# Optimization experiments

Measured on AMD Instinct MI355X. Metric: run time of the kernel, lower is better.

Reference implementation:

```python
import jax, jax.numpy as jnp
import numpy as np

NEG_SLOPE = 0.2  # PyG GATConv default negative_slope


def _gat_dense(x, W, att_src, att_dst, bias):
    """PyG GATConv on a fully-connected graph (self-loops included) == dense attention.
    x: [N, F_in], W: [F_in, H*C], att_src/att_dst: [H, C], bias: [H*C] or [C].
    Returns per-head outputs [N, H, C] (bias added by caller after concat/mean).
    """
    H, C = att_src.shape
    N = x.shape[0]
    h = (x @ W).reshape(N, H, C)                      # transformed node feats
    s = jnp.einsum('nhc,hc->nh', h, att_src)          # alpha_src per source node
    t = jnp.einsum('nhc,hc->nh', h, att_dst)          # alpha_dst per dest node
    # e[i, j, h] = leaky_relu(alpha_dst[i] + alpha_src[j]); softmax over sources j
    e = jax.nn.leaky_relu(t[:, None, :] + s[None, :, :], NEG_SLOPE)  # [N, N, H]
    a = jax.nn.softmax(e, axis=1)
    out = jnp.einsum('ijh,jhc->ihc', a, h)            # aggregate sources -> dest
    return out


def setup_inputs() -> dict:
    key = jax.random.key(0)
    ks = jax.random.split(key, 11)
    N, D, C, H = 4096, 768, 128, 4
    sd1 = 1.0 / np.sqrt(D)
    sd2 = 1.0 / np.sqrt(H * C)
    sd3 = 1.0 / np.sqrt(C)
    return {
        'node_feats': jax.random.normal(ks[0], (N, D), dtype=jnp.float32),
        'W1': jax.random.normal(ks[1], (D, H * C), dtype=jnp.float32) * sd1,
        'att_src1': jax.random.normal(ks[2], (H, C), dtype=jnp.float32) * sd3,
        'att_dst1': jax.random.normal(ks[3], (H, C), dtype=jnp.float32) * sd3,
        'b1': jnp.zeros((H * C,), dtype=jnp.float32),
        'W2': jax.random.normal(ks[4], (H * C, C), dtype=jnp.float32) * sd2,
        'att_src2': jax.random.normal(ks[5], (1, C), dtype=jnp.float32) * sd3,
        'att_dst2': jax.random.normal(ks[6], (1, C), dtype=jnp.float32) * sd3,
        'b2': jnp.zeros((C,), dtype=jnp.float32),
        'fcW': jax.random.normal(ks[7], (C, D), dtype=jnp.float32) * sd3,
        'fcb': jnp.zeros((D,), dtype=jnp.float32),
    }


def reference(node_feats, W1, att_src1, att_dst1, b1, W2, att_src2, att_dst2, b2, fcW, fcb):
    N = node_feats.shape[0]
    # GAT layer 1: 4 heads, concat=True
    x = _gat_dense(node_feats, W1, att_src1, att_dst1, b1).reshape(N, -1) + b1
    x = jax.nn.elu(x)
    # GAT layer 2: 1 head, concat=False (mean over the single head == identity)
    x = _gat_dense(x, W2, att_src2, att_dst2, b2)[:, 0, :] + b2
    x = jax.nn.elu(x)
    x = x.mean(axis=0)            # [gat_hidden]
    return x @ fcW + fcb          # [hidden_dim]
```

## Files before the change

kernel.cpp:

```cpp
#include <hip/hip_runtime.h>
#include <hip/hip_bf16.h>


#define NNODE 4096
#define CDIM 128
#define TW 132
#define NEG 0.2f
#define CHUNK 32
#define NCHUNK 128

typedef __bf16 bf16x8 __attribute__((ext_vector_type(8)));
typedef float f32x4 __attribute__((ext_vector_type(4)));

__device__ __forceinline__ unsigned short f2b(float f) {
  unsigned int u = __float_as_uint(f);
  u += 0x7fffu + ((u >> 16) & 1u);
  return (unsigned short)(u >> 16);
}

__global__ __launch_bounds__(256) void prep_kernel(const float* __restrict__ x,
                                                   const float* __restrict__ W1,
                                                   const float* __restrict__ W2,
                                                   unsigned short* __restrict__ xb,
                                                   unsigned short* __restrict__ W1t,
                                                   unsigned short* __restrict__ W2t,
                                                   float* __restrict__ zs1,
                                                   float* __restrict__ zs2) {
  __shared__ float tile[64][65];
  int b = blockIdx.x, t = threadIdx.x;
  if (b < 3072) {
    int i = b * 256 + t;
    float4 v = ((const float4*)x)[i];
    ushort4 o;
    o.x = f2b(v.x); o.y = f2b(v.y); o.z = f2b(v.z); o.w = f2b(v.w);
    ((ushort4*)xb)[i] = o;
    return;
  }
  if (b >= 3184) {
    float4 z = {0.f, 0.f, 0.f, 0.f};
    if (b < 3216) {
      ((float4*)zs1)[(b - 3184) * 256 + t] = z;
    } else {
      ((float4*)zs2)[(b - 3216) * 256 + t] = z;
    }
    return;
  }
  const float* W; unsigned short* Wt; int K, N, n0, k0;
  if (b < 3072 + 96) {
    int b2 = b - 3072; W = W1; Wt = W1t; K = 768; N = 512;
    n0 = (b2 & 7) * 64; k0 = (b2 >> 3) * 64;
  } else {
    int b3 = b - 3072 - 96; W = W2; Wt = W2t; K = 512; N = 128;
    n0 = (b3 & 1) * 64; k0 = (b3 >> 1) * 64;
  }
  for (int p = 0; p < 16; p++) {
    int e = p * 256 + t;
    int rr = e >> 6, cc = e & 63;
    tile[rr][cc] = W[(size_t)(k0 + rr) * N + n0 + cc];
  }
  __syncthreads();
  for (int p = 0; p < 16; p++) {
    int e = p * 256 + t;
    int rr = e >> 6, cc = e & 63;
    Wt[(size_t)(n0 + rr) * K + k0 + cc] = f2b(tile[cc][rr]);
  }
}

template <int BM, int BN>
__global__ __launch_bounds__(256) void mfma_gemm_bt(const unsigned short* __restrict__ A,
                                                    const unsigned short* __restrict__ Bt,
                                                    float* __restrict__ C,
                                                    int M, int N, int K,
                                                    float* __restrict__ sAcc,
                                                    float* __restrict__ tAcc,
                                                    const float* __restrict__ av_s,
                                                    const float* __restrict__ av_d) {
  __shared__ __align__(16) unsigned short As[BM * 40];
  __shared__ __align__(16) unsigned short Bs[BN * 40];
  constexpr int WM = BM / 2, WN = BN / 2;
  constexpr int FI = WM / 16, FJ = WN / 16;
  constexpr int EA = BM * 32 / 8;
  constexpr int EB = BN * 32 / 8;
  constexpr int NA = (EA + 255) / 256;
  constexpr int NB = (EB + 255) / 256;
  int tid = threadIdx.x;
  int lane = tid & 63, wave = tid >> 6;
  int wm = (wave >> 1) * WM, wn = (wave & 1) * WN;
  int m0 = blockIdx.y * BM, n0 = blockIdx.x * BN;
  int fm = lane & 15, fq = lane >> 4;
  f32x4 acc[FI][FJ] = {};
  uint4 ar[NA], br[NB];
#pragma unroll
  for (int q = 0; q < NA; q++) {
    int e = q * 256 + tid;
    if (e < EA) {
      int r = e >> 2, kk = (e & 3) * 8;
      ar[q] = *(const uint4*)(A + (size_t)(m0 + r) * K + kk);
    }
  }
#pragma unroll
  for (int q = 0; q < NB; q++) {
    int e = q * 256 + tid;
    if (e < EB) {
      int r = e >> 2, kk = (e & 3) * 8;
      br[q] = *(const uint4*)(Bt + (size_t)(n0 + r) * K + kk);
    }
  }
  for (int k0 = 0; k0 < K; k0 += 32) {
    __syncthreads();
#pragma unroll
    for (int q = 0; q < NA; q++) {
      int e = q * 256 + tid;
      if (e < EA) {
        int r = e >> 2, kk = (e & 3) * 8;
        *(uint4*)&As[r * 40 + kk] = ar[q];
      }
    }
#pragma unroll
    for (int q = 0; q < NB; q++) {
      int e = q * 256 + tid;
      if (e < EB) {
        int r = e >> 2, kk = (e & 3) * 8;
        *(uint4*)&Bs[r * 40 + kk] = br[q];
      }
    }
    __syncthreads();
    if (k0 + 32 < K) {
#pragma unroll
      for (int q = 0; q < NA; q++) {
        int e = q * 256 + tid;
        if (e < EA) {
          int r = e >> 2, kk = (e & 3) * 8;
          ar[q] = *(const uint4*)(A + (size_t)(m0 + r) * K + k0 + 32 + kk);
        }
      }
#pragma unroll
      for (int q = 0; q < NB; q++) {
        int e = q * 256 + tid;
        if (e < EB) {
          int r = e >> 2, kk = (e & 3) * 8;
          br[q] = *(const uint4*)(Bt + (size_t)(n0 + r) * K + k0 + 32 + kk);
        }
      }
    }
    bf16x8 af[FI], bfr[FJ];
#pragma unroll
    for (int i = 0; i < FI; i++)
      af[i] = *(const bf16x8*)&As[(wm + i * 16 + fm) * 40 + fq * 8];
#pragma unroll
    for (int j = 0; j < FJ; j++)
      bfr[j] = *(const bf16x8*)&Bs[(wn + j * 16 + fm) * 40 + fq * 8];
#pragma unroll
    for (int i = 0; i < FI; i++)
#pragma unroll
      for (int j = 0; j < FJ; j++)
        acc[i][j] = __builtin_amdgcn_mfma_f32_16x16x32_bf16(af[i], bfr[j], acc[i][j], 0, 0, 0);
  }
#pragma unroll
  for (int i = 0; i < FI; i++) {
#pragma unroll
    for (int j = 0; j < FJ; j++) {
      int r = m0 + wm + i * 16 + fq * 4;
      int ccol = n0 + wn + j * 16 + fm;
#pragma unroll
      for (int reg = 0; reg < 4; reg++)
        C[(size_t)(r + reg) * N + ccol] = acc[i][j][reg];
    }
  }
  {
    int hh = n0 >> 7;
    float avs[FJ], avd[FJ];
#pragma unroll
    for (int j = 0; j < FJ; j++) {
      int col = n0 + wn + j * 16 + fm;
      avs[j] = av_s[col];
      avd[j] = av_d[col];
    }
#pragma unroll
    for (int i = 0; i < FI; i++) {
#pragma unroll
      for (int reg = 0; reg < 4; reg++) {
        float sv = 0.f, tv = 0.f;
#pragma unroll
        for (int j = 0; j < FJ; j++) {
          sv = fmaf(acc[i][j][reg], avs[j], sv);
          tv = fmaf(acc[i][j][reg], avd[j], tv);
        }
#pragma unroll
        for (int o = 1; o < 16; o <<= 1) {
          sv += __shfl_xor(sv, o, 64);
          tv += __shfl_xor(tv, o, 64);
        }
        if (fm == 0) {
          int row = m0 + wm + i * 16 + fq * 4 + reg;
          atomicAdd(&sAcc[(size_t)hh * NNODE + row], sv);
          atomicAdd(&tAcc[(size_t)hh * NNODE + row], tv);
        }
      }
    }
  }
}

__global__ __launch_bounds__(256) void rank_sort_kernel(const float* __restrict__ s,
                                                        const float* __restrict__ t,
                                                        float* __restrict__ ss,
                                                        int* __restrict__ si,
                                                        int* __restrict__ qlo) {
  __shared__ __align__(16) float keys[NNODE];
  __shared__ int pc[8][32], qc[8][32];
  int hh = blockIdx.y, tid = threadIdx.x;
  const float* sp = s + (size_t)hh * NNODE;
  for (int k = tid; k < NNODE / 4; k += 256)
    ((float4*)keys)[k] = ((const float4*)sp)[k];
  __syncthreads();
  int slot = tid & 31, part = tid >> 5;
  int node = blockIdx.x * 32 + slot;
  float mk = keys[node];
  float qk = -t[(size_t)hh * NNODE + node];
  int cnt = 0, cq = 0;
  int j0 = part * 512;
#pragma unroll 4
  for (int j = j0; j < j0 + 512; j += 4) {
    float4 kv = *(const float4*)&keys[j];
    cnt += (kv.x < mk) || (kv.x == mk && (j + 0) < node);
    cnt += (kv.y < mk) || (kv.y == mk && (j + 1) < node);
    cnt += (kv.z < mk) || (kv.z == mk && (j + 2) < node);
    cnt += (kv.w < mk) || (kv.w == mk && (j + 3) < node);
    cq += (kv.x < qk) + (kv.y < qk) + (kv.z < qk) + (kv.w < qk);
  }
  pc[part][slot] = cnt;
  qc[part][slot] = cq;
  __syncthreads();
  if (tid < 32) {
    int rank = 0;
#pragma unroll
    for (int p = 0; p < 8; p++) rank += pc[p][tid];
    int n2 = blockIdx.x * 32 + tid;
    ss[(size_t)hh * NNODE + rank] = keys[n2];
    si[(size_t)hh * NNODE + rank] = n2;
  } else if (tid < 64) {
    int sl = tid - 32;
    int lo = 0;
#pragma unroll
    for (int p = 0; p < 8; p++) lo += qc[p][sl];
    qlo[(size_t)hh * NNODE + blockIdx.x * 32 + sl] = lo;
  }
}

__global__ __launch_bounds__(128) void passA_kernel(const float* __restrict__ h,
                                                    const float* __restrict__ ss,
                                                    const int* __restrict__ si,
                                                    float* __restrict__ partP,
                                                    float* __restrict__ partM, int H) {
  __shared__ float eP[CHUNK], eM[CHUNK];
  __shared__ int ids[CHUNK];
  int b = blockIdx.x, hh = b / NCHUNK, ci = b % NCHUNK;
  int c = threadIdx.x;
  int HC = H * CDIM;
  int base = ci * CHUNK;
  if (c < CHUNK) {
    float sv = ss[(size_t)hh * NNODE + base + c];
    ids[c] = si[(size_t)hh * NNODE + base + c];
    eP[c] = expf(sv);
    eM[c] = expf(NEG * sv);
  }
  __syncthreads();
  float sp = 0.f, sm = 0.f;
  for (int kb = 0; kb < CHUNK; kb += 8) {
    float v[8];
#pragma unroll
    for (int j = 0; j < 8; j++)
      v[j] = h[(size_t)ids[kb + j] * HC + hh * CDIM + c];
#pragma unroll
    for (int j = 0; j < 8; j++) {
      sp = fmaf(eP[kb + j], v[j], sp);
      sm = fmaf(eM[kb + j], v[j], sm);
    }
  }
  size_t o = ((size_t)hh * NCHUNK + ci) * TW;
  partP[o + c] = sp;
  partM[o + c] = sm;
  if (c == 0) {
    float zp = 0.f, zm = 0.f;
#pragma unroll
    for (int k = 0; k < CHUNK; k++) { zp += eP[k]; zm += eM[k]; }
    partP[o + 128] = zp;
    partM[o + 128] = zm;
  }
}

__global__ __launch_bounds__(192) void passB_kernel(const float* __restrict__ partP,
                                                    const float* __restrict__ partM,
                                                    float* __restrict__ sufP,
                                                    float* __restrict__ prefM) {
  int hh = blockIdx.y, dir = blockIdx.x;
  int c = threadIdx.x;
  if (c > 128) return;
  size_t base = (size_t)hh * NCHUNK * TW;
  if (dir == 0) {
    float run = 0.f;
    for (int g0 = 0; g0 < NCHUNK; g0 += 8) {
      float v[8];
#pragma unroll
      for (int j = 0; j < 8; j++) v[j] = partM[base + (size_t)(g0 + j) * TW + c];
#pragma unroll
      for (int j = 0; j < 8; j++) {
        prefM[base + (size_t)(g0 + j) * TW + c] = run;
        run += v[j];
      }
    }
  } else {
    float run = 0.f;
    for (int g0 = NCHUNK - 8; g0 >= 0; g0 -= 8) {
      float v[8];
#pragma unroll
      for (int j = 7; j >= 0; j--) v[j] = partP[base + (size_t)(g0 + j) * TW + c];
#pragma unroll
      for (int j = 7; j >= 0; j--) {
        sufP[base + (size_t)(g0 + j) * TW + c] = run;
        run += v[j];
      }
    }
  }
}

__global__ __launch_bounds__(128) void passC_kernel(const float* __restrict__ h,
                                                    const float* __restrict__ ss,
                                                    const int* __restrict__ si,
                                                    const float* __restrict__ sufP,
                                                    const float* __restrict__ prefM,
                                                    float* __restrict__ SS,
                                                    float* __restrict__ PP, int H) {
  __shared__ float hrow[CHUNK][CDIM];
  __shared__ float eP[CHUNK], eM[CHUNK];
  __shared__ int ids[CHUNK];
  int b = blockIdx.x, hh = b / NCHUNK, ci = b % NCHUNK;
  int c = threadIdx.x;
  int HC = H * CDIM;
  int base = ci * CHUNK;
  size_t hb = (size_t)hh * (NNODE + 1);
  if (c < CHUNK) {
    float sv = ss[(size_t)hh * NNODE + base + c];
    ids[c] = si[(size_t)hh * NNODE + base + c];
    eP[c] = expf(sv);
    eM[c] = expf(NEG * sv);
  }
  __syncthreads();
  size_t co = ((size_t)hh * NCHUNK + ci) * TW;
  float cm = prefM[co + c];
  float cp = sufP[co + c];
  float zcm = 0.f, zcp = 0.f;
  if (c == 0) { zcm = prefM[co + 128]; zcp = sufP[co + 128]; }
  for (int kb = 0; kb < CHUNK; kb += 8) {
    float v[8];
#pragma unroll
    for (int j = 0; j < 8; j++)
      v[j] = h[(size_t)ids[kb + j] * HC + hh * CDIM + c];
#pragma unroll
    for (int j = 0; j < 8; j++) hrow[kb + j][c] = v[j];
  }
  float runm = cm, runzm = zcm;
#pragma unroll 8
  for (int k = 0; k < CHUNK; k++) {
    size_t row = (hb + base + k) * TW;
    PP[row + c] = runm;
    if (c == 0) PP[row + 128] = runzm;
    runm = fmaf(eM[k], hrow[k][c], runm);
    runzm += eM[k];
  }
  if (ci == NCHUNK - 1) {
    size_t row = (hb + NNODE) * TW;
    PP[row + c] = runm;
    if (c == 0) PP[row + 128] = runzm;
  }
  float runp = cp, runzp = zcp;
#pragma unroll 8
  for (int k = CHUNK - 1; k >= 0; k--) {
    runp = fmaf(eP[k], hrow[k][c], runp);
    runzp += eP[k];
    size_t row = (hb + base + k) * TW;
    SS[row + c] = runp;
    if (c == 0) SS[row + 128] = runzp;
  }
  if (ci == NCHUNK - 1) {
    size_t row = (hb + NNODE) * TW;
    SS[row + c] = 0.f;
    if (c == 0) SS[row + 128] = 0.f;
  }
}

template <typename OUT>
__global__ __launch_bounds__(128) void attend_kernel(const float* __restrict__ SS,
                                                     const float* __restrict__ PP,
                                                     const int* __restrict__ qlo,
                                                     const float* __restrict__ tt,
                                                     const float* __restrict__ bias,
                                                     OUT* __restrict__ out, int H) {
  int b = blockIdx.x;
  int n = b / H, hh = b % H;
  int c = threadIdx.x;
  float tv = tt[(size_t)hh * NNODE + n];
  int lo = qlo[(size_t)hh * NNODE + n];
  size_t hb = (size_t)hh * (NNODE + 1);
  float wp = expf(tv), wm = expf(NEG * tv);
  float num = wp * SS[(hb + lo) * TW + c] + wm * PP[(hb + lo) * TW + c];
  float Z = wp * SS[(hb + lo) * TW + 128] + wm * PP[(hb + lo) * TW + 128];
  float o = num / Z + bias[hh * CDIM + c];
  float r = (o > 0.f) ? o : (expf(o) - 1.f);
  if constexpr (sizeof(OUT) == 2)
    out[(size_t)n * (H * CDIM) + hh * CDIM + c] = f2b(r);
  else
    out[(size_t)n * (H * CDIM) + hh * CDIM + c] = r;
}

__global__ __launch_bounds__(256) void mean_part_kernel(const float* __restrict__ x,
                                                        float* __restrict__ part) {
  __shared__ float4 red[256];
  int b = blockIdx.x, tid = threadIdx.x;
  int q = tid & 31, r0 = tid >> 5;
  const float4* xp = (const float4*)x;
  float4 s = {0.f, 0.f, 0.f, 0.f};
  int base = b * 64;
  for (int r = r0; r < 64; r += 8) {
    float4 v = xp[(size_t)(base + r) * 32 + q];
    s.x += v.x; s.y += v.y; s.z += v.z; s.w += v.w;
  }
  red[tid] = s; __syncthreads();
  for (int off = 4; off > 0; off >>= 1) {
    if (r0 < off) {
      float4 o = red[tid + off * 32];
      red[tid].x += o.x; red[tid].y += o.y; red[tid].z += o.z; red[tid].w += o.w;
    }
    __syncthreads();
  }
  if (tid < 32) ((float4*)part)[b * 32 + tid] = red[tid];
}

__global__ __launch_bounds__(256) void fc_kernel(const float* __restrict__ part,
                                                 const float* __restrict__ fcW,
                                                 const float* __restrict__ fcb,
                                                 float* __restrict__ out) {
  __shared__ float tmp[256];
  __shared__ float m[CDIM];
  int tid = threadIdx.x;
  int c = tid & 127, half = tid >> 7;
  float a = 0.f;
  for (int g = half; g < 64; g += 2) a += part[g * CDIM + c];
  tmp[tid] = a; __syncthreads();
  if (tid < 128) m[tid] = (tmp[tid] + tmp[tid + 128]) * (1.f / NNODE);
  __syncthreads();
  int d = blockIdx.x * 256 + tid;
  float acc = fcb[d];
#pragma unroll 4
  for (int c2 = 0; c2 < CDIM; c2++) acc = fmaf(m[c2], fcW[c2 * 768 + d], acc);
  out[d] = acc;
}

extern "C" void kernel_launch(void* const* d_in, const int* in_sizes, int n_in,
                              void* d_out, int out_size, void* d_ws, size_t ws_size,
                              hipStream_t stream) {
  const float* x   = (const float*)d_in[0];
  const float* W1  = (const float*)d_in[1];
  const float* as1 = (const float*)d_in[2];
  const float* ad1 = (const float*)d_in[3];
  const float* b1  = (const float*)d_in[4];
  const float* W2  = (const float*)d_in[5];
  const float* as2 = (const float*)d_in[6];
  const float* ad2 = (const float*)d_in[7];
  const float* b2  = (const float*)d_in[8];
  const float* fcW = (const float*)d_in[9];
  const float* fcb = (const float*)d_in[10];

  float* ws = (float*)d_ws;
  size_t off = 0;
  auto alloc = [&](size_t nfloats) { float* p = ws + off; off += nfloats; return p; };

  float* h1  = alloc((size_t)NNODE * 512);
  float* x2f = alloc((size_t)NNODE * 256 + 64 + 16384);
  float* h2  = alloc((size_t)NNODE * 128);
  float* x3  = alloc((size_t)NNODE * 128);
  float* s1  = alloc((size_t)4 * NNODE);
  float* t1  = alloc((size_t)4 * NNODE);
  float* sS1 = alloc((size_t)4 * NNODE);
  int*   sI1 = (int*)alloc((size_t)4 * NNODE);
  int*   qL1 = (int*)alloc((size_t)4 * NNODE);
  float* SS1 = alloc((size_t)4 * (NNODE + 1) * TW);
  float* PP1 = alloc((size_t)4 * (NNODE + 1) * TW);
  float* pP1 = alloc((size_t)4 * NCHUNK * TW);
  float* pM1 = alloc((size_t)4 * NCHUNK * TW);
  float* fP1 = alloc((size_t)4 * NCHUNK * TW);
  float* fM1 = alloc((size_t)4 * NCHUNK * TW);
  float* s2  = alloc(NNODE);
  float* t2  = alloc(NNODE);
  float* sS2 = alloc(NNODE);
  int*   sI2 = (int*)alloc(NNODE);
  int*   qL2 = (int*)alloc(NNODE);
  float* SS2 = alloc((size_t)(NNODE + 1) * TW);
  float* PP2 = alloc((size_t)(NNODE + 1) * TW);
  float* pP2 = alloc((size_t)NCHUNK * TW);
  float* pM2 = alloc((size_t)NCHUNK * TW);
  float* fP2 = alloc((size_t)NCHUNK * TW);
  float* fM2 = alloc((size_t)NCHUNK * TW);
  float* mpart = alloc((size_t)64 * CDIM);

  unsigned short* xb  = (unsigned short*)PP1;
  unsigned short* W1t = (unsigned short*)SS1;
  unsigned short* x2b = (unsigned short*)x2f;
  unsigned short* W2t = (unsigned short*)(x2f + NNODE * 256 + 64);

  prep_kernel<<<3224, 256, 0, stream>>>(x, W1, W2, xb, W1t, W2t, s1, s2);
  mfma_gemm_bt<64, 64><<<dim3(512 / 64, NNODE / 64), 256, 0, stream>>>(
      xb, W1t, h1, NNODE, 512, 768, s1, t1, as1, ad1);
  rank_sort_kernel<<<dim3(NNODE / 32, 4), 256, 0, stream>>>(s1, t1, sS1, sI1, qL1);
  passA_kernel<<<4 * NCHUNK, 128, 0, stream>>>(h1, sS1, sI1, pP1, pM1, 4);
  passB_kernel<<<dim3(2, 4), 192, 0, stream>>>(pP1, pM1, fP1, fM1);
  passC_kernel<<<4 * NCHUNK, 128, 0, stream>>>(h1, sS1, sI1, fP1, fM1, SS1, PP1, 4);
  attend_kernel<unsigned short><<<NNODE * 4, 128, 0, stream>>>(SS1, PP1, qL1, t1, b1, x2b, 4);
  mfma_gemm_bt<32, 64><<<dim3(128 / 64, NNODE / 32), 256, 0, stream>>>(
      x2b, W2t, h2, NNODE, 128, 512, s2, t2, as2, ad2);
  rank_sort_kernel<<<dim3(NNODE / 32, 1), 256, 0, stream>>>(s2, t2, sS2, sI2, qL2);
  passA_kernel<<<NCHUNK, 128, 0, stream>>>(h2, sS2, sI2, pP2, pM2, 1);
  passB_kernel<<<dim3(2, 1), 192, 0, stream>>>(pP2, pM2, fP2, fM2);
  passC_kernel<<<NCHUNK, 128, 0, stream>>>(h2, sS2, sI2, fP2, fM2, SS2, PP2, 1);
  attend_kernel<float><<<NNODE, 128, 0, stream>>>(SS2, PP2, qL2, t2, b2, x3, 1);
  mean_part_kernel<<<64, 256, 0, stream>>>(x3, mpart);
  fc_kernel<<<3, 256, 0, stream>>>(mpart, fcW, fcb, (float*)d_out);
}
```

Measured before the change: 209.6 us.

## Fuse per-layer attention stages into one cooperative kernel with grid syncs

Replaces the separate rank-sort, pass A/B/C, attend, mean and fc launches of each GAT layer with a single cooperative kernel of 512 blocks that uses grid.sync between stages and a shared-memory union. The aim is to remove many small kernel launches and their gaps. Work is also repacked into 256-thread blocks: pass A handles two chunks per block, pass C splits the prefix and suffix scans across half-blocks, and attend loops over several nodes per block. In exchange, idle blocks have to wait at grid barriers. The fixed 512-block grid must be fully co-resident for the cooperative launch to run.

```diff
diff --git a/kernel.cpp b/kernel.cpp
--- a/kernel.cpp
+++ b/kernel.cpp
@@ -1,5 +1,8 @@
 #include <hip/hip_runtime.h>
 #include <hip/hip_bf16.h>
+#include <hip/hip_cooperative_groups.h>
+
+namespace cg = cooperative_groups;
 
 
 #define NNODE 4096
@@ -8,6 +11,7 @@
 #define NEG 0.2f
 #define CHUNK 32
 #define NCHUNK 128
+#define CGRID 512
 
 typedef __bf16 bf16x8 __attribute__((ext_vector_type(8)));
 typedef float f32x4 __attribute__((ext_vector_type(4)));
@@ -201,259 +205,256 @@
   }
 }
 
-__global__ __launch_bounds__(256) void rank_sort_kernel(const float* __restrict__ s,
-                                                        const float* __restrict__ t,
-                                                        float* __restrict__ ss,
-                                                        int* __restrict__ si,
-                                                        int* __restrict__ qlo) {
-  __shared__ __align__(16) float keys[NNODE];
-  __shared__ int pc[8][32], qc[8][32];
-  int hh = blockIdx.y, tid = threadIdx.x;
-  const float* sp = s + (size_t)hh * NNODE;
-  for (int k = tid; k < NNODE / 4; k += 256)
-    ((float4*)keys)[k] = ((const float4*)sp)[k];
-  __syncthreads();
-  int slot = tid & 31, part = tid >> 5;
-  int node = blockIdx.x * 32 + slot;
-  float mk = keys[node];
-  float qk = -t[(size_t)hh * NNODE + node];
-  int cnt = 0, cq = 0;
-  int j0 = part * 512;
+struct SmSort { float keys[NNODE]; int pc[8][32]; int qc[8][32]; };
+struct SmA    { float eP[2][CHUNK]; float eM[2][CHUNK]; int ids[2][CHUNK]; };
+struct SmC    { float hrow[CHUNK][CDIM]; float eP[CHUNK]; float eM[CHUNK]; int ids[CHUNK]; };
+struct SmM    { float4 red[256]; };
+struct SmF    { float tmp[256]; float m[CDIM]; };
+union SmU { SmSort srt; SmA pa; SmC pc; SmM mp; SmF fc; };
+
+template <int H, typename OUT, bool READOUT>
+__global__ __launch_bounds__(256) void layer_coop(
+    const float* __restrict__ h,
+    const float* __restrict__ sv, const float* __restrict__ tvv,
+    float* __restrict__ ss, int* __restrict__ si, int* __restrict__ qlo,
+    float* __restrict__ pP, float* __restrict__ pM,
+    float* __restrict__ fP, float* __restrict__ fM,
+    float* __restrict__ SS, float* __restrict__ PP,
+    const float* __restrict__ bias, OUT* __restrict__ outp,
+    const float* __restrict__ fcW, const float* __restrict__ fcb,
+    float* __restrict__ mpart, float* __restrict__ fcout) {
+  __shared__ __align__(16) SmU sm;
+  cg::grid_group grid = cg::this_grid();
+  int b = blockIdx.x, tid = threadIdx.x;
+  constexpr int HC = H * CDIM;
+
+  if (b < H * 128) {
+    int hh = b >> 7, sb = b & 127;
+    const float* sp = sv + (size_t)hh * NNODE;
+    for (int k = tid; k < NNODE / 4; k += 256)
+      ((float4*)sm.srt.keys)[k] = ((const float4*)sp)[k];
+    __syncthreads();
+    int slot = tid & 31, part = tid >> 5;
+    int node = sb * 32 + slot;
+    float mk = sm.srt.keys[node];
+    float qk = -tvv[(size_t)hh * NNODE + node];
+    int cnt = 0, cq = 0;
+    int j0 = part * 512;
 #pragma unroll 4
-  for (int j = j0; j < j0 + 512; j += 4) {
-    float4 kv = *(const float4*)&keys[j];
-    cnt += (kv.x < mk) || (kv.x == mk && (j + 0) < node);
-    cnt += (kv.y < mk) || (kv.y == mk && (j + 1) < node);
-    cnt += (kv.z < mk) || (kv.z == mk && (j + 2) < node);
-    cnt += (kv.w < mk) || (kv.w == mk && (j + 3) < node);
-    cq += (kv.x < qk) + (kv.y < qk) + (kv.z < qk) + (kv.w < qk);
-  }
-  pc[part][slot] = cnt;
-  qc[part][slot] = cq;
-  __syncthreads();
-  if (tid < 32) {
-    int rank = 0;
-#pragma unroll
-    for (int p = 0; p < 8; p++) rank += pc[p][tid];
-    int n2 = blockIdx.x * 32 + tid;
-    ss[(size_t)hh * NNODE + rank] = keys[n2];
-    si[(size_t)hh * NNODE + rank] = n2;
-  } else if (tid < 64) {
-    int sl = tid - 32;
-    int lo = 0;
-#pragma unroll
-    for (int p = 0; p < 8; p++) lo += qc[p][sl];
-    qlo[(size_t)hh * NNODE + blockIdx.x * 32 + sl] = lo;
-  }
-}
-
-__global__ __launch_bounds__(128) void passA_kernel(const float* __restrict__ h,
-                                                    const float* __restrict__ ss,
-                                                    const int* __restrict__ si,
-                                                    float* __restrict__ partP,
-                                                    float* __restrict__ partM, int H) {
-  __shared__ float eP[CHUNK], eM[CHUNK];
-  __shared__ int ids[CHUNK];
-  int b = blockIdx.x, hh = b / NCHUNK, ci = b % NCHUNK;
-  int c = threadIdx.x;
-  int HC = H * CDIM;
-  int base = ci * CHUNK;
-  if (c < CHUNK) {
-    float sv = ss[(size_t)hh * NNODE + base + c];
-    ids[c] = si[(size_t)hh * NNODE + base + c];
-    eP[c] = expf(sv);
-    eM[c] = expf(NEG * sv);
-  }
-  __syncthreads();
-  float sp = 0.f, sm = 0.f;
-  for (int kb = 0; kb < CHUNK; kb += 8) {
-    float v[8];
-#pragma unroll
-    for (int j = 0; j < 8; j++)
-      v[j] = h[(size_t)ids[kb + j] * HC + hh * CDIM + c];
-#pragma unroll
-    for (int j = 0; j < 8; j++) {
-      sp = fmaf(eP[kb + j], v[j], sp);
-      sm = fmaf(eM[kb + j], v[j], sm);
-    }
-  }
-  size_t o = ((size_t)hh * NCHUNK + ci) * TW;
-  partP[o + c] = sp;
-  partM[o + c] = sm;
-  if (c == 0) {
-    float zp = 0.f, zm = 0.f;
-#pragma unroll
-    for (int k = 0; k < CHUNK; k++) { zp += eP[k]; zm += eM[k]; }
-    partP[o + 128] = zp;
-    partM[o + 128] = zm;
-  }
-}
-
-__global__ __launch_bounds__(192) void passB_kernel(const float* __restrict__ partP,
-                                                    const float* __restrict__ partM,
-                                                    float* __restrict__ sufP,
-                                                    float* __restrict__ prefM) {
-  int hh = blockIdx.y, dir = blockIdx.x;
-  int c = threadIdx.x;
-  if (c > 128) return;
-  size_t base = (size_t)hh * NCHUNK * TW;
-  if (dir == 0) {
-    float run = 0.f;
-    for (int g0 = 0; g0 < NCHUNK; g0 += 8) {
+    for (int j = j0; j < j0 + 512; j += 4) {
+      float4 kv = *(const float4*)&sm.srt.keys[j];
+      cnt += (kv.x < mk) || (kv.x == mk && (j + 0) < node);
+      cnt += (kv.y < mk) || (kv.y == mk && (j + 1) < node);
+      cnt += (kv.z < mk) || (kv.z == mk && (j + 2) < node);
+      cnt += (kv.w < mk) || (kv.w == mk && (j + 3) < node);
+      cq += (kv.x < qk) + (kv.y < qk) + (kv.z < qk) + (kv.w < qk);
+    }
+    sm.srt.pc[part][slot] = cnt;
+    sm.srt.qc[part][slot] = cq;
+    __syncthreads();
+    if (tid < 32) {
+      int rank = 0;
+#pragma unroll
+      for (int p = 0; p < 8; p++) rank += sm.srt.pc[p][tid];
+      int n2 = sb * 32 + tid;
+      ss[(size_t)hh * NNODE + rank] = sm.srt.keys[n2];
+      si[(size_t)hh * NNODE + rank] = n2;
+    } else if (tid < 64) {
+      int sl = tid - 32;
+      int lo = 0;
+#pragma unroll
+      for (int p = 0; p < 8; p++) lo += sm.srt.qc[p][sl];
+      qlo[(size_t)hh * NNODE + sb * 32 + sl] = lo;
+    }
+  }
+  grid.sync();
+
+  if (b < H * (NCHUNK / 2)) {
+    int half = tid >> 7, c = tid & 127;
+    int hh = b / (NCHUNK / 2), pair = b % (NCHUNK / 2);
+    int ci = pair * 2 + half;
+    int base = ci * CHUNK;
+    if (c < CHUNK) {
+      float s0 = ss[(size_t)hh * NNODE + base + c];
+      sm.pa.ids[half][c] = si[(size_t)hh * NNODE + base + c];
+      sm.pa.eP[half][c] = expf(s0);
+      sm.pa.eM[half][c] = expf(NEG * s0);
+    }
+    __syncthreads();
+    float sp = 0.f, smm = 0.f;
+    for (int kb = 0; kb < CHUNK; kb += 8) {
       float v[8];
 #pragma unroll
-      for (int j = 0; j < 8; j++) v[j] = partM[base + (size_t)(g0 + j) * TW + c];
+      for (int j = 0; j < 8; j++)
+        v[j] = h[(size_t)sm.pa.ids[half][kb + j] * HC + hh * CDIM + c];
 #pragma unroll
       for (int j = 0; j < 8; j++) {
-        prefM[base + (size_t)(g0 + j) * TW + c] = run;
-        run += v[j];
-      }
-    }
-  } else {
-    float run = 0.f;
-    for (int g0 = NCHUNK - 8; g0 >= 0; g0 -= 8) {
+        sp = fmaf(sm.pa.eP[half][kb + j], v[j], sp);
+        smm = fmaf(sm.pa.eM[half][kb + j], v[j], smm);
+      }
+    }
+    size_t o = ((size_t)hh * NCHUNK + ci) * TW;
+    pP[o + c] = sp;
+    pM[o + c] = smm;
+    if (c == 0) {
+      float zp = 0.f, zm = 0.f;
+#pragma unroll
+      for (int k = 0; k < CHUNK; k++) { zp += sm.pa.eP[half][k]; zm += sm.pa.eM[half][k]; }
+      pP[o + 128] = zp;
+      pM[o + 128] = zm;
+    }
+  }
+  grid.sync();
+
+  if (b < 2 * H && tid <= 128) {
+    int hh = b >> 1, dir = b & 1;
+    int c = tid;
+    size_t base = (size_t)hh * NCHUNK * TW;
+    if (dir == 0) {
+      float run = 0.f;
+      for (int g0 = 0; g0 < NCHUNK; g0 += 8) {
+        float v[8];
+#pragma unroll
+        for (int j = 0; j < 8; j++) v[j] = pM[base + (size_t)(g0 + j) * TW + c];
+#pragma unroll
+        for (int j = 0; j < 8; j++) {
+          fM[base + (size_t)(g0 + j) * TW + c] = run;
+          run += v[j];
+        }
+      }
+    } else {
+      float run = 0.f;
+      for (int g0 = NCHUNK - 8; g0 >= 0; g0 -= 8) {
+        float v[8];
+#pragma unroll
+        for (int j = 7; j >= 0; j--) v[j] = pP[base + (size_t)(g0 + j) * TW + c];
+#pragma unroll
+        for (int j = 7; j >= 0; j--) {
+          fP[base + (size_t)(g0 + j) * TW + c] = run;
+          run += v[j];
+        }
+      }
+    }
+  }
+  grid.sync();
+
+  if (b < H * NCHUNK) {
+    int hh = b / NCHUNK, ci = b % NCHUNK;
+    int c = tid & 127, half = tid >> 7;
+    int base = ci * CHUNK;
+    size_t hb = (size_t)hh * (NNODE + 1);
+    if (tid < CHUNK) {
+      float s0 = ss[(size_t)hh * NNODE + base + tid];
+      sm.pc.ids[tid] = si[(size_t)hh * NNODE + base + tid];
+      sm.pc.eP[tid] = expf(s0);
+      sm.pc.eM[tid] = expf(NEG * s0);
+    }
+    __syncthreads();
+    for (int kb = half * 16; kb < half * 16 + 16; kb += 8) {
       float v[8];
 #pragma unroll
-      for (int j = 7; j >= 0; j--) v[j] = partP[base + (size_t)(g0 + j) * TW + c];
-#pragma unroll
-      for (int j = 7; j >= 0; j--) {
-        sufP[base + (size_t)(g0 + j) * TW + c] = run;
-        run += v[j];
-      }
-    }
-  }
-}
-
-__global__ __launch_bounds__(128) void passC_kernel(const float* __restrict__ h,
-                                                    const float* __restrict__ ss,
-                                                    const int* __restrict__ si,
-                                                    const float* __restrict__ sufP,
-                                                    const float* __restrict__ prefM,
-                                                    float* __restrict__ SS,
-                                                    float* __restrict__ PP, int H) {
-  __shared__ float hrow[CHUNK][CDIM];
-  __shared__ float eP[CHUNK], eM[CHUNK];
-  __shared__ int ids[CHUNK];
-  int b = blockIdx.x, hh = b / NCHUNK, ci = b % NCHUNK;
-  int c = threadIdx.x;
-  int HC = H * CDIM;
-  int base = ci * CHUNK;
-  size_t hb = (size_t)hh * (NNODE + 1);
-  if (c < CHUNK) {
-    float sv = ss[(size_t)hh * NNODE + base + c];
-    ids[c] = si[(size_t)hh * NNODE + base + c];
-    eP[c] = expf(sv);
-    eM[c] = expf(NEG * sv);
-  }
-  __syncthreads();
-  size_t co = ((size_t)hh * NCHUNK + ci) * TW;
-  float cm = prefM[co + c];
-  float cp = sufP[co + c];
-  float zcm = 0.f, zcp = 0.f;
-  if (c == 0) { zcm = prefM[co + 128]; zcp = sufP[co + 128]; }
-  for (int kb = 0; kb < CHUNK; kb += 8) {
-    float v[8];
-#pragma unroll
-    for (int j = 0; j < 8; j++)
-      v[j] = h[(size_t)ids[kb + j] * HC + hh * CDIM + c];
-#pragma unroll
-    for (int j = 0; j < 8; j++) hrow[kb + j][c] = v[j];
-  }
-  float runm = cm, runzm = zcm;
+      for (int j = 0; j < 8; j++)
+        v[j] = h[(size_t)sm.pc.ids[kb + j] * HC + hh * CDIM + c];
+#pragma unroll
+      for (int j = 0; j < 8; j++) sm.pc.hrow[kb + j][c] = v[j];
+    }
+    __syncthreads();
+    size_t co = ((size_t)hh * NCHUNK + ci) * TW;
+    if (half == 0) {
+      float runm = fM[co + c];
+      float runzm = (c == 0) ? fM[co + 128] : 0.f;
 #pragma unroll 8
-  for (int k = 0; k < CHUNK; k++) {
-    size_t row = (hb + base + k) * TW;
-    PP[row + c] = runm;
-    if (c == 0) PP[row + 128] = runzm;
-    runm = fmaf(eM[k], hrow[k][c], runm);
-    runzm += eM[k];
-  }
-  if (ci == NCHUNK - 1) {
-    size_t row = (hb + NNODE) * TW;
-    PP[row + c] = runm;
-    if (c == 0) PP[row + 128] = runzm;
-  }
-  float runp = cp, runzp = zcp;
+      for (int k = 0; k < CHUNK; k++) {
+        size_t row = (hb + base + k) * TW;
+        PP[row + c] = runm;
+        if (c == 0) PP[row + 128] = runzm;
+        runm = fmaf(sm.pc.eM[k], sm.pc.hrow[k][c], runm);
+        runzm += sm.pc.eM[k];
+      }
+      if (ci == NCHUNK - 1) {
+        size_t row = (hb + NNODE) * TW;
+        PP[row + c] = runm;
+        if (c == 0) PP[row + 128] = runzm;
+      }
+    } else {
+      float runp = fP[co + c];
+      float runzp = (c == 0) ? fP[co + 128] : 0.f;
 #pragma unroll 8
-  for (int k = CHUNK - 1; k >= 0; k--) {
-    runp = fmaf(eP[k], hrow[k][c], runp);
-    runzp += eP[k];
-    size_t row = (hb + base + k) * TW;
-    SS[row + c] = runp;
-    if (c == 0) SS[row + 128] = runzp;
-  }
-  if (ci == NCHUNK - 1) {
-    size_t row = (hb + NNODE) * TW;
-    SS[row + c] = 0.f;
-    if (c == 0) SS[row + 128] = 0.f;
-  }
-}
-
-template <typename OUT>
-__global__ __launch_bounds__(128) void attend_kernel(const float* __restrict__ SS,
-                                                     const float* __restrict__ PP,
-                                                     const int* __restrict__ qlo,
-                                                     const float* __restrict__ tt,
-                                                     const float* __restrict__ bias,
-                                                     OUT* __restrict__ out, int H) {
-  int b = blockIdx.x;
-  int n = b / H, hh = b % H;
-  int c = threadIdx.x;
-  float tv = tt[(size_t)hh * NNODE + n];
-  int lo = qlo[(size_t)hh * NNODE + n];
-  size_t hb = (size_t)hh * (NNODE + 1);
-  float wp = expf(tv), wm = expf(NEG * tv);
-  float num = wp * SS[(hb + lo) * TW + c] + wm * PP[(hb + lo) * TW + c];
-  float Z = wp * SS[(hb + lo) * TW + 128] + wm * PP[(hb + lo) * TW + 128];
-  float o = num / Z + bias[hh * CDIM + c];
-  float r = (o > 0.f) ? o : (expf(o) - 1.f);
-  if constexpr (sizeof(OUT) == 2)
-    out[(size_t)n * (H * CDIM) + hh * CDIM + c] = f2b(r);
-  else
-    out[(size_t)n * (H * CDIM) + hh * CDIM + c] = r;
-}
-
-__global__ __launch_bounds__(256) void mean_part_kernel(const float* __restrict__ x,
-                                                        float* __restrict__ part) {
-  __shared__ float4 red[256];
-  int b = blockIdx.x, tid = threadIdx.x;
-  int q = tid & 31, r0 = tid >> 5;
-  const float4* xp = (const float4*)x;
-  float4 s = {0.f, 0.f, 0.f, 0.f};
-  int base = b * 64;
-  for (int r = r0; r < 64; r += 8) {
-    float4 v = xp[(size_t)(base + r) * 32 + q];
-    s.x += v.x; s.y += v.y; s.z += v.z; s.w += v.w;
-  }
-  red[tid] = s; __syncthreads();
-  for (int off = 4; off > 0; off >>= 1) {
-    if (r0 < off) {
-      float4 o = red[tid + off * 32];
-      red[tid].x += o.x; red[tid].y += o.y; red[tid].z += o.z; red[tid].w += o.w;
-    }
-    __syncthreads();
-  }
-  if (tid < 32) ((float4*)part)[b * 32 + tid] = red[tid];
-}
-
-__global__ __launch_bounds__(256) void fc_kernel(const float* __restrict__ part,
-                                                 const float* __restrict__ fcW,
-                                                 const float* __restrict__ fcb,
-                                                 float* __restrict__ out) {
-  __shared__ float tmp[256];
-  __shared__ float m[CDIM];
-  int tid = threadIdx.x;
-  int c = tid & 127, half = tid >> 7;
-  float a = 0.f;
-  for (int g = half; g < 64; g += 2) a += part[g * CDIM + c];
-  tmp[tid] = a; __syncthreads();
-  if (tid < 128) m[tid] = (tmp[tid] + tmp[tid + 128]) * (1.f / NNODE);
-  __syncthreads();
-  int d = blockIdx.x * 256 + tid;
-  float acc = fcb[d];
+      for (int k = CHUNK - 1; k >= 0; k--) {
+        runp = fmaf(sm.pc.eP[k], sm.pc.hrow[k][c], runp);
+        runzp += sm.pc.eP[k];
+        size_t row = (hb + base + k) * TW;
+        SS[row + c] = runp;
+        if (c == 0) SS[row + 128] = runzp;
+      }
+      if (ci == NCHUNK - 1) {
+        size_t row = (hb + NNODE) * TW;
+        SS[row + c] = 0.f;
+        if (c == 0) SS[row + 128] = 0.f;
+      }
+    }
+  }
+  grid.sync();
+
+  {
+    constexpr int PER = (H * NNODE) / CGRID;
+    int half = tid >> 7, c = tid & 127;
+#pragma unroll 2
+    for (int it = 0; it < PER / 2; it++) {
+      int o = b * PER + it * 2 + half;
+      int n = o / H, hh = o % H;
+      float tv = tvv[(size_t)hh * NNODE + n];
+      int lo = qlo[(size_t)hh * NNODE + n];
+      size_t hb = (size_t)hh * (NNODE + 1);
+      float wp = expf(tv), wm = expf(NEG * tv);
+      float num = wp * SS[(hb + lo) * TW + c] + wm * PP[(hb + lo) * TW + c];
+      float Z = wp * SS[(hb + lo) * TW + 128] + wm * PP[(hb + lo) * TW + 128];
+      float ov = num / Z + bias[hh * CDIM + c];
+      float r = (ov > 0.f) ? ov : (expf(ov) - 1.f);
+      if constexpr (sizeof(OUT) == 2)
+        outp[(size_t)n * HC + hh * CDIM + c] = f2b(r);
+      else
+        outp[(size_t)n * HC + hh * CDIM + c] = r;
+    }
+  }
+
+  if constexpr (READOUT) {
+    grid.sync();
+    if (b < 64) {
+      int q = tid & 31, r0 = tid >> 5;
+      const float4* xp = (const float4*)outp;
+      float4 s4 = {0.f, 0.f, 0.f, 0.f};
+      int base = b * 64;
+      for (int r = r0; r < 64; r += 8) {
+        float4 v = xp[(size_t)(base + r) * 32 + q];
+        s4.x += v.x; s4.y += v.y; s4.z += v.z; s4.w += v.w;
+      }
+      sm.mp.red[tid] = s4; __syncthreads();
+      for (int off = 4; off > 0; off >>= 1) {
+        if (r0 < off) {
+          float4 o4 = sm.mp.red[tid + off * 32];
+          sm.mp.red[tid].x += o4.x; sm.mp.red[tid].y += o4.y;
+          sm.mp.red[tid].z += o4.z; sm.mp.red[tid].w += o4.w;
+        }
+        __syncthreads();
+      }
+      if (tid < 32) ((float4*)mpart)[b * 32 + tid] = sm.mp.red[tid];
+    }
+    grid.sync();
+    if (b < 3) {
+      int c = tid & 127, hf = tid >> 7;
+      float a = 0.f;
+      for (int g = hf; g < 64; g += 2) a += mpart[g * CDIM + c];
+      sm.fc.tmp[tid] = a; __syncthreads();
+      if (tid < 128) sm.fc.m[tid] = (sm.fc.tmp[tid] + sm.fc.tmp[tid + 128]) * (1.f / NNODE);
+      __syncthreads();
+      int d = b * 256 + tid;
+      float acc = fcb[d];
 #pragma unroll 4
-  for (int c2 = 0; c2 < CDIM; c2++) acc = fmaf(m[c2], fcW[c2 * 768 + d], acc);
-  out[d] = acc;
+      for (int c2 = 0; c2 < CDIM; c2++) acc = fmaf(sm.fc.m[c2], fcW[c2 * 768 + d], acc);
+      fcout[d] = acc;
+    }
+  }
 }
 
 extern "C" void kernel_launch(void* const* d_in, const int* in_sizes, int n_in,
@@ -507,22 +508,27 @@
   unsigned short* W1t = (unsigned short*)SS1;
   unsigned short* x2b = (unsigned short*)x2f;
   unsigned short* W2t = (unsigned short*)(x2f + NNODE * 256 + 64);
+  float* dout = (float*)d_out;
 
   prep_kernel<<<3224, 256, 0, stream>>>(x, W1, W2, xb, W1t, W2t, s1, s2);
   mfma_gemm_bt<64, 64><<<dim3(512 / 64, NNODE / 64), 256, 0, stream>>>(
       xb, W1t, h1, NNODE, 512, 768, s1, t1, as1, ad1);
-  rank_sort_kernel<<<dim3(NNODE / 32, 4), 256, 0, stream>>>(s1, t1, sS1, sI1, qL1);
-  passA_kernel<<<4 * NCHUNK, 128, 0, stream>>>(h1, sS1, sI1, pP1, pM1, 4);
-  passB_kernel<<<dim3(2, 4), 192, 0, stream>>>(pP1, pM1, fP1, fM1);
-  passC_kernel<<<4 * NCHUNK, 128, 0, stream>>>(h1, sS1, sI1, fP1, fM1, SS1, PP1, 4);
-  attend_kernel<unsigned short><<<NNODE * 4, 128, 0, stream>>>(SS1, PP1, qL1, t1, b1, x2b, 4);
+  {
+    auto* kfn = layer_coop<4, unsigned short, false>;
+    void* ka[] = {(void*)&h1, (void*)&s1, (void*)&t1, (void*)&sS1, (void*)&sI1,
+                  (void*)&qL1, (void*)&pP1, (void*)&pM1, (void*)&fP1, (void*)&fM1,
+                  (void*)&SS1, (void*)&PP1, (void*)&b1, (void*)&x2b,
+                  (void*)&fcW, (void*)&fcb, (void*)&mpart, (void*)&dout};
+    hipLaunchCooperativeKernel((const void*)kfn, dim3(CGRID), dim3(256), ka, 0, stream);
+  }
   mfma_gemm_bt<32, 64><<<dim3(128 / 64, NNODE / 32), 256, 0, stream>>>(
       x2b, W2t, h2, NNODE, 128, 512, s2, t2, as2, ad2);
-  rank_sort_kernel<<<dim3(NNODE / 32, 1), 256, 0, stream>>>(s2, t2, sS2, sI2, qL2);
-  passA_kernel<<<NCHUNK, 128, 0, stream>>>(h2, sS2, sI2, pP2, pM2, 1);
-  passB_kernel<<<dim3(2, 1), 192, 0, stream>>>(pP2, pM2, fP2, fM2);
-  passC_kernel<<<NCHUNK, 128, 0, stream>>>(h2, sS2, sI2, fP2, fM2, SS2, PP2, 1);
-  attend_kernel<float><<<NNODE, 128, 0, stream>>>(SS2, PP2, qL2, t2, b2, x3, 1);
-  mean_part_kernel<<<64, 256, 0, stream>>>(x3, mpart);
-  fc_kernel<<<3, 256, 0, stream>>>(mpart, fcW, fcb, (float*)d_out);
+  {
+    auto* kfn = layer_coop<1, float, true>;
+    void* ka[] = {(void*)&h2, (void*)&s2, (void*)&t2, (void*)&sS2, (void*)&sI2,
+                  (void*)&qL2, (void*)&pP2, (void*)&pM2, (void*)&fP2, (void*)&fM2,
+                  (void*)&SS2, (void*)&PP2, (void*)&b2, (void*)&x3,
+                  (void*)&fcW, (void*)&fcb, (void*)&mpart, (void*)&dout};
+    hipLaunchCooperativeKernel((const void*)kfn, dim3(CGRID), dim3(256), ka, 0, stream);
+  }
 }
```

Result: slower. 753.6 us (+259.5%).

## Fuse chunk-local scans with partial sums and add chunk offsets in attend

Applied to the files above, without the earlier changes.

Merges passA and passC into one kernel. It writes chunk-local prefix and suffix scans together with the per-chunk totals, so the gather of h rows happens once instead of twice. The cross-chunk offsets from passB are now added inside attend_kernel, which reads two more small vectors per output. attend_kernel also processes two (node, head) pairs per 256-thread block, halving the block count. This removes a full kernel launch and a second gather pass, at the cost of extra loads in attend.

```diff
diff --git a/kernel.cpp b/kernel.cpp
--- a/kernel.cpp
+++ b/kernel.cpp
@@ -247,90 +247,13 @@
   }
 }
 
-__global__ __launch_bounds__(128) void passA_kernel(const float* __restrict__ h,
-                                                    const float* __restrict__ ss,
-                                                    const int* __restrict__ si,
-                                                    float* __restrict__ partP,
-                                                    float* __restrict__ partM, int H) {
-  __shared__ float eP[CHUNK], eM[CHUNK];
-  __shared__ int ids[CHUNK];
-  int b = blockIdx.x, hh = b / NCHUNK, ci = b % NCHUNK;
-  int c = threadIdx.x;
-  int HC = H * CDIM;
-  int base = ci * CHUNK;
-  if (c < CHUNK) {
-    float sv = ss[(size_t)hh * NNODE + base + c];
-    ids[c] = si[(size_t)hh * NNODE + base + c];
-    eP[c] = expf(sv);
-    eM[c] = expf(NEG * sv);
-  }
-  __syncthreads();
-  float sp = 0.f, sm = 0.f;
-  for (int kb = 0; kb < CHUNK; kb += 8) {
-    float v[8];
-#pragma unroll
-    for (int j = 0; j < 8; j++)
-      v[j] = h[(size_t)ids[kb + j] * HC + hh * CDIM + c];
-#pragma unroll
-    for (int j = 0; j < 8; j++) {
-      sp = fmaf(eP[kb + j], v[j], sp);
-      sm = fmaf(eM[kb + j], v[j], sm);
-    }
-  }
-  size_t o = ((size_t)hh * NCHUNK + ci) * TW;
-  partP[o + c] = sp;
-  partM[o + c] = sm;
-  if (c == 0) {
-    float zp = 0.f, zm = 0.f;
-#pragma unroll
-    for (int k = 0; k < CHUNK; k++) { zp += eP[k]; zm += eM[k]; }
-    partP[o + 128] = zp;
-    partM[o + 128] = zm;
-  }
-}
-
-__global__ __launch_bounds__(192) void passB_kernel(const float* __restrict__ partP,
-                                                    const float* __restrict__ partM,
-                                                    float* __restrict__ sufP,
-                                                    float* __restrict__ prefM) {
-  int hh = blockIdx.y, dir = blockIdx.x;
-  int c = threadIdx.x;
-  if (c > 128) return;
-  size_t base = (size_t)hh * NCHUNK * TW;
-  if (dir == 0) {
-    float run = 0.f;
-    for (int g0 = 0; g0 < NCHUNK; g0 += 8) {
-      float v[8];
-#pragma unroll
-      for (int j = 0; j < 8; j++) v[j] = partM[base + (size_t)(g0 + j) * TW + c];
-#pragma unroll
-      for (int j = 0; j < 8; j++) {
-        prefM[base + (size_t)(g0 + j) * TW + c] = run;
-        run += v[j];
-      }
-    }
-  } else {
-    float run = 0.f;
-    for (int g0 = NCHUNK - 8; g0 >= 0; g0 -= 8) {
-      float v[8];
-#pragma unroll
-      for (int j = 7; j >= 0; j--) v[j] = partP[base + (size_t)(g0 + j) * TW + c];
-#pragma unroll
-      for (int j = 7; j >= 0; j--) {
-        sufP[base + (size_t)(g0 + j) * TW + c] = run;
-        run += v[j];
-      }
-    }
-  }
-}
-
-__global__ __launch_bounds__(128) void passC_kernel(const float* __restrict__ h,
-                                                    const float* __restrict__ ss,
-                                                    const int* __restrict__ si,
-                                                    const float* __restrict__ sufP,
-                                                    const float* __restrict__ prefM,
-                                                    float* __restrict__ SS,
-                                                    float* __restrict__ PP, int H) {
+__global__ __launch_bounds__(128) void passAC_kernel(const float* __restrict__ h,
+                                                     const float* __restrict__ ss,
+                                                     const int* __restrict__ si,
+                                                     float* __restrict__ partP,
+                                                     float* __restrict__ partM,
+                                                     float* __restrict__ SS,
+                                                     float* __restrict__ PP, int H) {
   __shared__ float hrow[CHUNK][CDIM];
   __shared__ float eP[CHUNK], eM[CHUNK];
   __shared__ int ids[CHUNK];
@@ -346,11 +269,6 @@
     eM[c] = expf(NEG * sv);
   }
   __syncthreads();
-  size_t co = ((size_t)hh * NCHUNK + ci) * TW;
-  float cm = prefM[co + c];
-  float cp = sufP[co + c];
-  float zcm = 0.f, zcp = 0.f;
-  if (c == 0) { zcm = prefM[co + 128]; zcp = sufP[co + 128]; }
   for (int kb = 0; kb < CHUNK; kb += 8) {
     float v[8];
 #pragma unroll
@@ -359,7 +277,7 @@
 #pragma unroll
     for (int j = 0; j < 8; j++) hrow[kb + j][c] = v[j];
   }
-  float runm = cm, runzm = zcm;
+  float runm = 0.f, runzm = 0.f;
 #pragma unroll 8
   for (int k = 0; k < CHUNK; k++) {
     size_t row = (hb + base + k) * TW;
@@ -368,12 +286,15 @@
     runm = fmaf(eM[k], hrow[k][c], runm);
     runzm += eM[k];
   }
+  size_t o = ((size_t)hh * NCHUNK + ci) * TW;
+  partM[o + c] = runm;
+  if (c == 0) partM[o + 128] = runzm;
   if (ci == NCHUNK - 1) {
     size_t row = (hb + NNODE) * TW;
     PP[row + c] = runm;
     if (c == 0) PP[row + 128] = runzm;
   }
-  float runp = cp, runzp = zcp;
+  float runp = 0.f, runzp = 0.f;
 #pragma unroll 8
   for (int k = CHUNK - 1; k >= 0; k--) {
     runp = fmaf(eP[k], hrow[k][c], runp);
@@ -382,6 +303,8 @@
     SS[row + c] = runp;
     if (c == 0) SS[row + 128] = runzp;
   }
+  partP[o + c] = runp;
+  if (c == 0) partP[o + 128] = runzp;
   if (ci == NCHUNK - 1) {
     size_t row = (hb + NNODE) * TW;
     SS[row + c] = 0.f;
@@ -389,24 +312,66 @@
   }
 }
 
+__global__ __launch_bounds__(192) void passB_kernel(const float* __restrict__ partP,
+                                                    const float* __restrict__ partM,
+                                                    float* __restrict__ sufP,
+                                                    float* __restrict__ prefM) {
+  int hh = blockIdx.y, dir = blockIdx.x;
+  int c = threadIdx.x;
+  if (c > 128) return;
+  size_t base = (size_t)hh * NCHUNK * TW;
+  if (dir == 0) {
+    float run = 0.f;
+    for (int g0 = 0; g0 < NCHUNK; g0 += 8) {
+      float v[8];
+#pragma unroll
+      for (int j = 0; j < 8; j++) v[j] = partM[base + (size_t)(g0 + j) * TW + c];
+#pragma unroll
+      for (int j = 0; j < 8; j++) {
+        prefM[base + (size_t)(g0 + j) * TW + c] = run;
+        run += v[j];
+      }
+    }
+  } else {
+    float run = 0.f;
+    for (int g0 = NCHUNK - 8; g0 >= 0; g0 -= 8) {
+      float v[8];
+#pragma unroll
+      for (int j = 7; j >= 0; j--) v[j] = partP[base + (size_t)(g0 + j) * TW + c];
+#pragma unroll
+      for (int j = 7; j >= 0; j--) {
+        sufP[base + (size_t)(g0 + j) * TW + c] = run;
+        run += v[j];
+      }
+    }
+  }
+}
+
 template <typename OUT>
-__global__ __launch_bounds__(128) void attend_kernel(const float* __restrict__ SS,
+__global__ __launch_bounds__(256) void attend_kernel(const float* __restrict__ SS,
                                                      const float* __restrict__ PP,
+                                                     const float* __restrict__ fP,
+                                                     const float* __restrict__ fM,
                                                      const int* __restrict__ qlo,
                                                      const float* __restrict__ tt,
                                                      const float* __restrict__ bias,
                                                      OUT* __restrict__ out, int H) {
-  int b = blockIdx.x;
-  int n = b / H, hh = b % H;
-  int c = threadIdx.x;
+  int half = threadIdx.x >> 7, c = threadIdx.x & 127;
+  int o = blockIdx.x * 2 + half;
+  int n = o / H, hh = o % H;
   float tv = tt[(size_t)hh * NNODE + n];
   int lo = qlo[(size_t)hh * NNODE + n];
+  int ci = lo >> 5;
+  if (ci > NCHUNK - 1) ci = NCHUNK - 1;
   size_t hb = (size_t)hh * (NNODE + 1);
+  size_t co = ((size_t)hh * NCHUNK + ci) * TW;
   float wp = expf(tv), wm = expf(NEG * tv);
-  float num = wp * SS[(hb + lo) * TW + c] + wm * PP[(hb + lo) * TW + c];
-  float Z = wp * SS[(hb + lo) * TW + 128] + wm * PP[(hb + lo) * TW + 128];
-  float o = num / Z + bias[hh * CDIM + c];
-  float r = (o > 0.f) ? o : (expf(o) - 1.f);
+  float num = wp * (SS[(hb + lo) * TW + c] + fP[co + c]) +
+              wm * (PP[(hb + lo) * TW + c] + fM[co + c]);
+  float Z = wp * (SS[(hb + lo) * TW + 128] + fP[co + 128]) +
+            wm * (PP[(hb + lo) * TW + 128] + fM[co + 128]);
+  float ov = num / Z + bias[hh * CDIM + c];
+  float r = (ov > 0.f) ? ov : (expf(ov) - 1.f);
   if constexpr (sizeof(OUT) == 2)
     out[(size_t)n * (H * CDIM) + hh * CDIM + c] = f2b(r);
   else
@@ -512,17 +477,17 @@
   mfma_gemm_bt<64, 64><<<dim3(512 / 64, NNODE / 64), 256, 0, stream>>>(
       xb, W1t, h1, NNODE, 512, 768, s1, t1, as1, ad1);
   rank_sort_kernel<<<dim3(NNODE / 32, 4), 256, 0, stream>>>(s1, t1, sS1, sI1, qL1);
-  passA_kernel<<<4 * NCHUNK, 128, 0, stream>>>(h1, sS1, sI1, pP1, pM1, 4);
+  passAC_kernel<<<4 * NCHUNK, 128, 0, stream>>>(h1, sS1, sI1, pP1, pM1, SS1, PP1, 4);
   passB_kernel<<<dim3(2, 4), 192, 0, stream>>>(pP1, pM1, fP1, fM1);
-  passC_kernel<<<4 * NCHUNK, 128, 0, stream>>>(h1, sS1, sI1, fP1, fM1, SS1, PP1, 4);
-  attend_kernel<unsigned short><<<NNODE * 4, 128, 0, stream>>>(SS1, PP1, qL1, t1, b1, x2b, 4);
+  attend_kernel<unsigned short><<<NNODE * 4 / 2, 256, 0, stream>>>(
+      SS1, PP1, fP1, fM1, qL1, t1, b1, x2b, 4);
   mfma_gemm_bt<32, 64><<<dim3(128 / 64, NNODE / 32), 256, 0, stream>>>(
       x2b, W2t, h2, NNODE, 128, 512, s2, t2, as2, ad2);
   rank_sort_kernel<<<dim3(NNODE / 32, 1), 256, 0, stream>>>(s2, t2, sS2, sI2, qL2);
-  passA_kernel<<<NCHUNK, 128, 0, stream>>>(h2, sS2, sI2, pP2, pM2, 1);
+  passAC_kernel<<<NCHUNK, 128, 0, stream>>>(h2, sS2, sI2, pP2, pM2, SS2, PP2, 1);
   passB_kernel<<<dim3(2, 1), 192, 0, stream>>>(pP2, pM2, fP2, fM2);
-  passC_kernel<<<NCHUNK, 128, 0, stream>>>(h2, sS2, sI2, fP2, fM2, SS2, PP2, 1);
-  attend_kernel<float><<<NNODE, 128, 0, stream>>>(SS2, PP2, qL2, t2, b2, x3, 1);
+  attend_kernel<float><<<NNODE / 2, 256, 0, stream>>>(
+      SS2, PP2, fP2, fM2, qL2, t2, b2, x3, 1);
   mean_part_kernel<<<64, 256, 0, stream>>>(x3, mpart);
   fc_kernel<<<3, 256, 0, stream>>>(mpart, fcW, fcb, (float*)d_out);
 }
```

Result: faster. 204.0 us (-2.7%).
